# Optimization experiments

Hardware: AMD Instinct MI355X
Metric: run time of the kernel (lower is better)

## Reference

```python
import jax, jax.numpy as jnp
import numpy as np

N_NODES = 50000
N_EDGES = 800000
IN_CH = 128
HID = 32
HEADS = 8
OUT_CH = 40
NEG_SLOPE = 0.2


def setup_inputs() -> dict:
    key = jax.random.key(0)
    ks = jax.random.split(key, 12)
    g = lambda k, shape, fan: (jax.random.normal(k, shape, jnp.float32) / np.sqrt(fan).astype(np.float32))
    return {
        "x": jax.random.normal(ks[0], (N_NODES, IN_CH), jnp.float32),
        "edge_index": jax.random.randint(ks[1], (2, N_EDGES), 0, N_NODES, jnp.int64),
        "W1l": g(ks[2], (IN_CH, HEADS * HID), IN_CH),
        "W1r": g(ks[3], (IN_CH, HEADS * HID), IN_CH),
        "att1": g(ks[4], (HEADS, HID), HID),
        "b1": jnp.zeros((HEADS * HID,), jnp.float32),
        "W2l": g(ks[5], (HEADS * HID, HID), HEADS * HID),
        "W2r": g(ks[6], (HEADS * HID, HID), HEADS * HID),
        "att2": g(ks[7], (1, HID), HID),
        "b2": jnp.zeros((HID,), jnp.float32),
        "Wc": g(ks[8], (HID + IN_CH, OUT_CH), HID + IN_CH),
        "bc": jnp.zeros((OUT_CH,), jnp.float32),
    }


def _gatv2(x, ei, Wl, Wr, att, b, heads, ch):
    # GATv2Conv (concat=True): e_ij = att . LeakyReLU(Wl x_j + Wr x_i)
    n = x.shape[0]
    src, dst = ei[0], ei[1]  # message flows src(j) -> dst(i)
    xl = (x @ Wl).reshape(n, heads, ch)  # source transform
    xr = (x @ Wr).reshape(n, heads, ch)  # target transform
    e = jax.nn.leaky_relu(xl[src] + xr[dst], NEG_SLOPE)  # [E, H, C]
    score = jnp.einsum("ehc,hc->eh", e, att)             # [E, H]
    # per-target-node segment softmax (stable)
    m = jax.ops.segment_max(score, dst, num_segments=n)
    alpha = jnp.exp(score - m[dst])
    denom = jax.ops.segment_sum(alpha, dst, num_segments=n)
    alpha = alpha / denom[dst]
    out = jax.ops.segment_sum(alpha[:, :, None] * xl[src], dst, num_segments=n)
    return out.reshape(n, heads * ch) + b


def reference(x, edge_index, W1l, W1r, att1, b1, W2l, W2r, att2, b2, Wc, bc):
    n = x.shape[0]
    ar = jnp.arange(n, dtype=edge_index.dtype)
    ei = jnp.concatenate([edge_index, jnp.stack([ar, ar])], axis=1)  # add self-loops
    h1 = jax.nn.elu(_gatv2(x, ei, W1l, W1r, att1, b1, HEADS, HID))
    h2 = jax.nn.elu(_gatv2(h1, ei, W2l, W2r, att2, b2, 1, HID))
    combined = jnp.concatenate([h2, x], axis=1)
    return combined @ Wc + bc
```

## Files before the change

kernel.cpp:

```cpp
#include <hip/hip_runtime.h>
#include <cstdint>
#include <cstddef>
#include <math.h>

#define NN 50000
#define INCH 128
#define HIDC 32
#define NHEAD 8
#define OUTC 40

typedef unsigned short ushort_t;
using bf16x8 = __attribute__((ext_vector_type(8))) short;
using f32x4  = __attribute__((ext_vector_type(4))) float;

__device__ __forceinline__ float bf2f(unsigned short h) {
    return __uint_as_float(((unsigned int)h) << 16);
}
__device__ __forceinline__ unsigned short f2bf(float f) {
    unsigned int u = __float_as_uint(f);
    u = u + 0x7FFFu + ((u >> 16) & 1u);
    return (unsigned short)(u >> 16);
}
__device__ __forceinline__ float lo16(unsigned int u) { return __uint_as_float(u << 16); }
__device__ __forceinline__ float hi16(unsigned int u) { return __uint_as_float(u & 0xffff0000u); }

__global__ __launch_bounds__(256) void prep_all(
    const float* __restrict__ x, ushort_t* __restrict__ xb, int total8,
    const float* __restrict__ W1l, const float* __restrict__ W1r,
    const float* __restrict__ W2l, const float* __restrict__ W2r,
    const float* __restrict__ Wc,
    ushort_t* __restrict__ BT1, ushort_t* __restrict__ BT2, ushort_t* __restrict__ BTc,
    const int* __restrict__ ei, int E, int n, int* __restrict__ deg, int CX) {
    const int blk = blockIdx.x;
    const int tid = threadIdx.x;
    if (blk < CX) {
        int i = blk * 256 + tid;
        if (i >= total8) return;
        float4 f0 = *(const float4*)(x + (size_t)i * 8);
        float4 f1 = *(const float4*)(x + (size_t)i * 8 + 4);
        ushort4 u0, u1;
        u0.x = f2bf(f0.x); u0.y = f2bf(f0.y); u0.z = f2bf(f0.z); u0.w = f2bf(f0.w);
        u1.x = f2bf(f1.x); u1.y = f2bf(f1.y); u1.z = f2bf(f1.z); u1.w = f2bf(f1.w);
        *(ushort4*)(xb + (size_t)i * 8) = u0;
        *(ushort4*)(xb + (size_t)i * 8 + 4) = u1;
    } else if (blk < CX + 616) {
        int b = blk - CX, k = tid;
        if (b < 512) {
            if (k < 128) {
                float v = (b < 256) ? W1l[(size_t)k * 256 + b] : W1r[(size_t)k * 256 + (b - 256)];
                BT1[(size_t)b * 128 + k] = f2bf(v);
            }
        } else if (b < 576) {
            int c = b - 512;
            float v = (c < 32) ? W2l[(size_t)k * 32 + c] : W2r[(size_t)k * 32 + (c - 32)];
            BT2[(size_t)c * 256 + k] = f2bf(v);
        } else {
            int c = b - 576;
            if (k < 160) BTc[(size_t)c * 160 + k] = f2bf(Wc[(size_t)k * 40 + c]);
        }
    } else {
        int e = (blk - CX - 616) * 256 + tid;
        if (e >= E + n) return;
        int dst = (e < E) ? ei[E + e] : (e - E);
        atomicAdd(&deg[dst], 1);
    }
}


__global__ __launch_bounds__(1024) void partial_scan(
    const int* __restrict__ deg, int* __restrict__ row_start,
    int* __restrict__ block_total, int n) {
    __shared__ int wsum[16];
    const int tid = threadIdx.x, lane = tid & 63, wid = tid >> 6;
    int i = blockIdx.x * 1024 + tid;
    int v = (i < n) ? deg[i] : 0;
    int s = v;
    #pragma unroll
    for (int off = 1; off < 64; off <<= 1) {
        int t = __shfl_up(s, off, 64);
        if (lane >= off) s += t;
    }
    if (lane == 63) wsum[wid] = s;
    __syncthreads();
    if (wid == 0) {
        int ws = (lane < 16) ? wsum[lane] : 0;
        #pragma unroll
        for (int off = 1; off < 16; off <<= 1) {
            int t = __shfl_up(ws, off, 64);
            if (lane >= off) ws += t;
        }
        if (lane < 16) wsum[lane] = ws;
    }
    __syncthreads();
    int wexcl = wid ? wsum[wid - 1] : 0;
    if (i < n) row_start[i] = wexcl + s - v;
    if (tid == 0) block_total[blockIdx.x] = wsum[15];
}

__global__ void totals_scan(const int* __restrict__ block_total, int* __restrict__ block_off,
                            int* __restrict__ row_start_n, int nb) {
    int j = threadIdx.x;
    int v = (j < nb) ? block_total[j] : 0;
    int s = v;
    #pragma unroll
    for (int off = 1; off < 64; off <<= 1) {
        int t = __shfl_up(s, off, 64);
        if (j >= off) s += t;
    }
    if (j < nb) block_off[j] = s - v;
    if (j == nb - 1) *row_start_n = s;
}

__global__ __launch_bounds__(1024) void add_off(int* __restrict__ row_start, int* __restrict__ cursor,
                                                const int* __restrict__ block_off, int n) {
    int i = blockIdx.x * 1024 + threadIdx.x;
    if (i >= n) return;
    int val = row_start[i] + block_off[blockIdx.x];
    row_start[i] = val;
    cursor[i] = val;
}

__global__ void scatter_edges(const int* __restrict__ ei, int E, int n,
                              int* __restrict__ cursor, int* __restrict__ csr_src) {
    int e = blockIdx.x * blockDim.x + threadIdx.x;
    if (e >= E + n) return;
    int src, dst;
    if (e < E) { src = ei[e]; dst = ei[E + e]; } else { src = dst = e - E; }
    int pos = atomicAdd(&cursor[dst], 1);
    csr_src[pos] = src;
}

__global__ __launch_bounds__(256) void gemm1_mfma(
    const ushort_t* __restrict__ xb, const ushort_t* __restrict__ BT1,
    const float* __restrict__ att,
    ushort_t* __restrict__ xlr1, float* __restrict__ dl, float* __restrict__ dr, int M) {
    __shared__ ushort_t As[128][72];
    __shared__ ushort_t Bs[128][72];
    const int tid = threadIdx.x;
    const int rowBase = blockIdx.y * 128;
    const int bx = blockIdx.x;
    const int c0 = bx * 128;
    const int wid = tid >> 6, lane = tid & 63;
    const int wr = wid >> 1, wc = wid & 1;
    const int l15 = lane & 15, l4 = lane >> 4;
    f32x4 acc[4][4];
    #pragma unroll
    for (int i = 0; i < 4; ++i)
        #pragma unroll
        for (int j = 0; j < 4; ++j)
            #pragma unroll
            for (int q = 0; q < 4; ++q) acc[i][j][q] = 0.f;

    for (int c = 0; c < 2; ++c) {
        #pragma unroll
        for (int h = 0; h < 4; ++h) {
            int idx = h * 256 + tid;
            int r = idx >> 3, seg = idx & 7;
            int row = rowBase + r;
            uint4 v = {0, 0, 0, 0};
            if (row < M) v = *(const uint4*)(xb + (size_t)row * 128 + c * 64 + seg * 8);
            *(uint4*)&As[r][seg * 8] = v;
            *(uint4*)&Bs[r][seg * 8] = *(const uint4*)(BT1 + (size_t)(c0 + r) * 128 + c * 64 + seg * 8);
        }
        __syncthreads();
        #pragma unroll
        for (int kk = 0; kk < 2; ++kk) {
            bf16x8 a[4], b[4];
            #pragma unroll
            for (int f = 0; f < 4; ++f) {
                a[f] = *(const bf16x8*)&As[wr * 64 + f * 16 + l15][kk * 32 + l4 * 8];
                b[f] = *(const bf16x8*)&Bs[wc * 64 + f * 16 + l15][kk * 32 + l4 * 8];
            }
            #pragma unroll
            for (int i = 0; i < 4; ++i)
                #pragma unroll
                for (int j = 0; j < 4; ++j)
                    acc[i][j] = __builtin_amdgcn_mfma_f32_16x16x32_bf16(a[i], b[j], acc[i][j], 0, 0, 0);
        }
        __syncthreads();
    }
    #pragma unroll
    for (int i = 0; i < 4; ++i)
        #pragma unroll
        for (int r = 0; r < 4; ++r) {
            int row = rowBase + wr * 64 + i * 16 + l4 * 4 + r;
            if (row >= M) continue;
            #pragma unroll
            for (int j = 0; j < 4; ++j) {
                int col = c0 + wc * 64 + j * 16 + l15;
                xlr1[(size_t)row * 512 + col] = f2bf(acc[i][j][r]);
            }
        }
    float attv[4];
    #pragma unroll
    for (int j = 0; j < 4; ++j)
        attv[j] = att[(bx & 1) * 128 + wc * 64 + j * 16 + l15];
    float* __restrict__ dst = (bx < 2) ? dl : dr;
    const int headA = (bx & 1) * 4 + wc * 2;
    #pragma unroll
    for (int i = 0; i < 4; ++i)
        #pragma unroll
        for (int r = 0; r < 4; ++r) {
            float s0 = fmaf(acc[i][1][r], attv[1], acc[i][0][r] * attv[0]);
            float s1 = fmaf(acc[i][3][r], attv[3], acc[i][2][r] * attv[2]);
            s0 += __shfl_xor(s0, 1); s1 += __shfl_xor(s1, 1);
            s0 += __shfl_xor(s0, 2); s1 += __shfl_xor(s1, 2);
            s0 += __shfl_xor(s0, 4); s1 += __shfl_xor(s1, 4);
            s0 += __shfl_xor(s0, 8); s1 += __shfl_xor(s1, 8);
            if (l15 == 0) {
                int row = rowBase + wr * 64 + i * 16 + l4 * 4 + r;
                if (row < M) {
                    dst[(size_t)row * 8 + headA] = s0;
                    dst[(size_t)row * 8 + headA + 1] = s1;
                }
            }
        }
}

__global__ __launch_bounds__(256) void gat_agg1(
    const ushort_t* __restrict__ xlr, const float* __restrict__ dl,
    const float* __restrict__ dr, const float* __restrict__ att,
    const float* __restrict__ b,
    const int* __restrict__ row_start, const int* __restrict__ csr_src,
    ushort_t* __restrict__ h1) {
    const int lane = threadIdx.x & 63;
    const int i = blockIdx.x * 4 + (threadIdx.x >> 6);
    const int half = lane >> 5;
    const int sl = lane & 31;
    const int head = sl >> 2;

    uint4 xv = *(const uint4*)(xlr + (size_t)i * 512 + 256 + sl * 8);
    const float xr0 = lo16(xv.x), xr1 = hi16(xv.x), xr2 = lo16(xv.y), xr3 = hi16(xv.y);
    const float xr4 = lo16(xv.z), xr5 = hi16(xv.z), xr6 = lo16(xv.w), xr7 = hi16(xv.w);
    const float4 atA = *(const float4*)(att + sl * 8);
    const float4 atB = *(const float4*)(att + sl * 8 + 4);
    const float cbase = 0.6f * dr[(size_t)i * 8 + head];
    const int p0 = row_start[i], p1 = row_start[i + 1];

    float d = 0.f;
    float a0 = 0.f, a1 = 0.f, a2 = 0.f, a3 = 0.f, a4 = 0.f, a5 = 0.f, a6 = 0.f, a7 = 0.f;

    int e0 = p0 + half;     int pc0 = e0 < p1 ? e0 : p1 - 1;
    int j0 = csr_src[pc0];
    uint4 uv0 = *(const uint4*)(xlr + (size_t)j0 * 512 + sl * 8);
    float dl0 = dl[(size_t)j0 * 8 + head];
    int e1 = p0 + half + 2; int pc1 = e1 < p1 ? e1 : p1 - 1;
    int j1 = csr_src[pc1];
    uint4 uv1 = *(const uint4*)(xlr + (size_t)j1 * 512 + sl * 8);
    float dl1 = dl[(size_t)j1 * 8 + head];

    for (int p = p0; p < p1; p += 4) {
        {
            const bool val = (p + half) < p1;
            float v0 = lo16(uv0.x), v1 = hi16(uv0.x), v2 = lo16(uv0.y), v3 = hi16(uv0.y);
            float v4 = lo16(uv0.z), v5 = hi16(uv0.z), v6 = lo16(uv0.w), v7 = hi16(uv0.w);
            float base = fmaf(0.6f, dl0, cbase);
            int nxt = p + half + 4;
            if (nxt < p1) {
                int jn = csr_src[nxt];
                uv0 = *(const uint4*)(xlr + (size_t)jn * 512 + sl * 8);
                dl0 = dl[(size_t)jn * 8 + head];
            }
            float q = atA.x * fabsf(v0 + xr0);
            q = fmaf(atA.y, fabsf(v1 + xr1), q);
            q = fmaf(atA.z, fabsf(v2 + xr2), q);
            q = fmaf(atA.w, fabsf(v3 + xr3), q);
            q = fmaf(atB.x, fabsf(v4 + xr4), q);
            q = fmaf(atB.y, fabsf(v5 + xr5), q);
            q = fmaf(atB.z, fabsf(v6 + xr6), q);
            q = fmaf(atB.w, fabsf(v7 + xr7), q);
            q += __shfl_xor(q, 1);
            q += __shfl_xor(q, 2);
            float w = val ? __expf(fmaf(0.4f, q, base)) : 0.f;
            d += w;
            a0 = fmaf(w, v0, a0); a1 = fmaf(w, v1, a1);
            a2 = fmaf(w, v2, a2); a3 = fmaf(w, v3, a3);
            a4 = fmaf(w, v4, a4); a5 = fmaf(w, v5, a5);
            a6 = fmaf(w, v6, a6); a7 = fmaf(w, v7, a7);
        }
        {
            const bool val = (p + 2 + half) < p1;
            float v0 = lo16(uv1.x), v1 = hi16(uv1.x), v2 = lo16(uv1.y), v3 = hi16(uv1.y);
            float v4 = lo16(uv1.z), v5 = hi16(uv1.z), v6 = lo16(uv1.w), v7 = hi16(uv1.w);
            float base = fmaf(0.6f, dl1, cbase);
            int nxt = p + half + 6;
            if (nxt < p1) {
                int jn = csr_src[nxt];
                uv1 = *(const uint4*)(xlr + (size_t)jn * 512 + sl * 8);
                dl1 = dl[(size_t)jn * 8 + head];
            }
            float q = atA.x * fabsf(v0 + xr0);
            q = fmaf(atA.y, fabsf(v1 + xr1), q);
            q = fmaf(atA.z, fabsf(v2 + xr2), q);
            q = fmaf(atA.w, fabsf(v3 + xr3), q);
            q = fmaf(atB.x, fabsf(v4 + xr4), q);
            q = fmaf(atB.y, fabsf(v5 + xr5), q);
            q = fmaf(atB.z, fabsf(v6 + xr6), q);
            q = fmaf(atB.w, fabsf(v7 + xr7), q);
            q += __shfl_xor(q, 1);
            q += __shfl_xor(q, 2);
            float w = val ? __expf(fmaf(0.4f, q, base)) : 0.f;
            d += w;
            a0 = fmaf(w, v0, a0); a1 = fmaf(w, v1, a1);
            a2 = fmaf(w, v2, a2); a3 = fmaf(w, v3, a3);
            a4 = fmaf(w, v4, a4); a5 = fmaf(w, v5, a5);
            a6 = fmaf(w, v6, a6); a7 = fmaf(w, v7, a7);
        }
    }
    d  += __shfl_xor(d, 32);
    a0 += __shfl_xor(a0, 32); a1 += __shfl_xor(a1, 32);
    a2 += __shfl_xor(a2, 32); a3 += __shfl_xor(a3, 32);
    a4 += __shfl_xor(a4, 32); a5 += __shfl_xor(a5, 32);
    a6 += __shfl_xor(a6, 32); a7 += __shfl_xor(a7, 32);

    if (half == 0) {
        const float4 bA = *(const float4*)(b + sl * 8);
        const float4 bB = *(const float4*)(b + sl * 8 + 4);
        float inv = 1.f / d;
        float o0 = fmaf(a0, inv, bA.x), o1 = fmaf(a1, inv, bA.y);
        float o2 = fmaf(a2, inv, bA.z), o3 = fmaf(a3, inv, bA.w);
        float o4 = fmaf(a4, inv, bB.x), o5 = fmaf(a5, inv, bB.y);
        float o6 = fmaf(a6, inv, bB.z), o7 = fmaf(a7, inv, bB.w);
        o0 = o0 > 0.f ? o0 : __expf(o0) - 1.f;
        o1 = o1 > 0.f ? o1 : __expf(o1) - 1.f;
        o2 = o2 > 0.f ? o2 : __expf(o2) - 1.f;
        o3 = o3 > 0.f ? o3 : __expf(o3) - 1.f;
        o4 = o4 > 0.f ? o4 : __expf(o4) - 1.f;
        o5 = o5 > 0.f ? o5 : __expf(o5) - 1.f;
        o6 = o6 > 0.f ? o6 : __expf(o6) - 1.f;
        o7 = o7 > 0.f ? o7 : __expf(o7) - 1.f;
        uint4 ov;
        ov.x = ((unsigned)f2bf(o1) << 16) | f2bf(o0);
        ov.y = ((unsigned)f2bf(o3) << 16) | f2bf(o2);
        ov.z = ((unsigned)f2bf(o5) << 16) | f2bf(o4);
        ov.w = ((unsigned)f2bf(o7) << 16) | f2bf(o6);
        *(uint4*)(h1 + (size_t)i * 256 + sl * 8) = ov;
    }
}

__global__ __launch_bounds__(256) void gemm2_mfma(
    const ushort_t* __restrict__ h1, const ushort_t* __restrict__ BT2,
    const float* __restrict__ att,
    ushort_t* __restrict__ xlr2, float* __restrict__ dl2, float* __restrict__ dr2, int M) {
    __shared__ ushort_t As[128][72];
    __shared__ ushort_t Bs[64][264];
    const int tid = threadIdx.x;
    const int rowBase = blockIdx.x * 128;
    const int wid = tid >> 6, lane = tid & 63;
    const int l15 = lane & 15, l4 = lane >> 4;
    #pragma unroll
    for (int h = 0; h < 8; ++h) {
        int idx = h * 256 + tid;
        int r = idx >> 5, seg = idx & 31;
        *(uint4*)&Bs[r][seg * 8] = *(const uint4*)(BT2 + (size_t)r * 256 + seg * 8);
    }
    f32x4 acc[2][4];
    #pragma unroll
    for (int i = 0; i < 2; ++i)
        #pragma unroll
        for (int j = 0; j < 4; ++j)
            #pragma unroll
            for (int q = 0; q < 4; ++q) acc[i][j][q] = 0.f;

    for (int c = 0; c < 4; ++c) {
        #pragma unroll
        for (int h = 0; h < 4; ++h) {
            int idx = h * 256 + tid;
            int r = idx >> 3, seg = idx & 7;
            int row = rowBase + r;
            uint4 v = {0, 0, 0, 0};
            if (row < M) v = *(const uint4*)(h1 + (size_t)row * 256 + c * 64 + seg * 8);
            *(uint4*)&As[r][seg * 8] = v;
        }
        __syncthreads();
        #pragma unroll
        for (int kk = 0; kk < 2; ++kk) {
            bf16x8 a[2], b[4];
            #pragma unroll
            for (int f = 0; f < 2; ++f)
                a[f] = *(const bf16x8*)&As[wid * 32 + f * 16 + l15][kk * 32 + l4 * 8];
            #pragma unroll
            for (int f = 0; f < 4; ++f)
                b[f] = *(const bf16x8*)&Bs[f * 16 + l15][c * 64 + kk * 32 + l4 * 8];
            #pragma unroll
            for (int i = 0; i < 2; ++i)
                #pragma unroll
                for (int j = 0; j < 4; ++j)
                    acc[i][j] = __builtin_amdgcn_mfma_f32_16x16x32_bf16(a[i], b[j], acc[i][j], 0, 0, 0);
        }
        __syncthreads();
    }
    #pragma unroll
    for (int i = 0; i < 2; ++i)
        #pragma unroll
        for (int r = 0; r < 4; ++r) {
            int row = rowBase + wid * 32 + i * 16 + l4 * 4 + r;
            if (row >= M) continue;
            #pragma unroll
            for (int j = 0; j < 4; ++j) {
                int col = j * 16 + l15;
                xlr2[(size_t)row * 64 + col] = f2bf(acc[i][j][r]);
            }
        }
    float attv[4];
    #pragma unroll
    for (int j = 0; j < 4; ++j)
        attv[j] = att[(j * 16 + l15) & 31];
    #pragma unroll
    for (int i = 0; i < 2; ++i)
        #pragma unroll
        for (int r = 0; r < 4; ++r) {
            float s0 = fmaf(acc[i][1][r], attv[1], acc[i][0][r] * attv[0]);
            float s1 = fmaf(acc[i][3][r], attv[3], acc[i][2][r] * attv[2]);
            s0 += __shfl_xor(s0, 1); s1 += __shfl_xor(s1, 1);
            s0 += __shfl_xor(s0, 2); s1 += __shfl_xor(s1, 2);
            s0 += __shfl_xor(s0, 4); s1 += __shfl_xor(s1, 4);
            s0 += __shfl_xor(s0, 8); s1 += __shfl_xor(s1, 8);
            if (l15 == 0) {
                int row = rowBase + wid * 32 + i * 16 + l4 * 4 + r;
                if (row < M) {
                    dl2[row] = s0;
                    dr2[row] = s1;
                }
            }
        }
}

__global__ __launch_bounds__(256) void gat_agg2(
    const ushort_t* __restrict__ xlr, const float* __restrict__ dl,
    const float* __restrict__ dr, const float* __restrict__ att,
    const float* __restrict__ b,
    const int* __restrict__ row_start, const int* __restrict__ csr_src,
    ushort_t* __restrict__ h2) {
    const int lane = threadIdx.x & 63;
    const int i = blockIdx.x * 4 + (threadIdx.x >> 6);
    const int g = lane >> 3;
    const int h8 = lane & 7;
    uint2 xv = *(const uint2*)(xlr + (size_t)i * 64 + 32 + h8 * 4);
    const float xr0 = lo16(xv.x), xr1 = hi16(xv.x), xr2 = lo16(xv.y), xr3 = hi16(xv.y);
    const float4 at = *(const float4*)(att + h8 * 4);
    const float cbase = 0.6f * dr[i];
    const int p0 = row_start[i], p1 = row_start[i + 1];
    float d = 0.f, a0 = 0.f, a1 = 0.f, a2 = 0.f, a3 = 0.f;

    int e0 = p0 + g;     int pc0 = e0 < p1 ? e0 : p1 - 1;
    int j0 = csr_src[pc0];
    uint2 uv0 = *(const uint2*)(xlr + (size_t)j0 * 64 + h8 * 4);
    float dl0 = dl[j0];
    int e1 = p0 + g + 8; int pc1 = e1 < p1 ? e1 : p1 - 1;
    int j1 = csr_src[pc1];
    uint2 uv1 = *(const uint2*)(xlr + (size_t)j1 * 64 + h8 * 4);
    float dl1 = dl[j1];

    for (int p = p0; p < p1; p += 16) {
        {
            const bool val = (p + g) < p1;
            float v0 = lo16(uv0.x), v1 = hi16(uv0.x), v2 = lo16(uv0.y), v3 = hi16(uv0.y);
            float base = fmaf(0.6f, dl0, cbase);
            int nxt = p + g + 16;
            if (nxt < p1) {
                int jn = csr_src[nxt];
                uv0 = *(const uint2*)(xlr + (size_t)jn * 64 + h8 * 4);
                dl0 = dl[jn];
            }
            float q = at.x * fabsf(v0 + xr0);
            q = fmaf(at.y, fabsf(v1 + xr1), q);
            q = fmaf(at.z, fabsf(v2 + xr2), q);
            q = fmaf(at.w, fabsf(v3 + xr3), q);
            q += __shfl_xor(q, 1);
            q += __shfl_xor(q, 2);
            q += __shfl_xor(q, 4);
            float w = val ? __expf(fmaf(0.4f, q, base)) : 0.f;
            d += w;
            a0 = fmaf(w, v0, a0); a1 = fmaf(w, v1, a1);
            a2 = fmaf(w, v2, a2); a3 = fmaf(w, v3, a3);
        }
        {
            const bool val = (p + g + 8) < p1;
            float v0 = lo16(uv1.x), v1 = hi16(uv1.x), v2 = lo16(uv1.y), v3 = hi16(uv1.y);
            float base = fmaf(0.6f, dl1, cbase);
            int nxt = p + g + 24;
            if (nxt < p1) {
                int jn = csr_src[nxt];
                uv1 = *(const uint2*)(xlr + (size_t)jn * 64 + h8 * 4);
                dl1 = dl[jn];
            }
            float q = at.x * fabsf(v0 + xr0);
            q = fmaf(at.y, fabsf(v1 + xr1), q);
            q = fmaf(at.z, fabsf(v2 + xr2), q);
            q = fmaf(at.w, fabsf(v3 + xr3), q);
            q += __shfl_xor(q, 1);
            q += __shfl_xor(q, 2);
            q += __shfl_xor(q, 4);
            float w = val ? __expf(fmaf(0.4f, q, base)) : 0.f;
            d += w;
            a0 = fmaf(w, v0, a0); a1 = fmaf(w, v1, a1);
            a2 = fmaf(w, v2, a2); a3 = fmaf(w, v3, a3);
        }
    }
    d  += __shfl_xor(d, 8);  d  += __shfl_xor(d, 16);  d  += __shfl_xor(d, 32);
    a0 += __shfl_xor(a0, 8); a0 += __shfl_xor(a0, 16); a0 += __shfl_xor(a0, 32);
    a1 += __shfl_xor(a1, 8); a1 += __shfl_xor(a1, 16); a1 += __shfl_xor(a1, 32);
    a2 += __shfl_xor(a2, 8); a2 += __shfl_xor(a2, 16); a2 += __shfl_xor(a2, 32);
    a3 += __shfl_xor(a3, 8); a3 += __shfl_xor(a3, 16); a3 += __shfl_xor(a3, 32);
    if (g == 0) {
        const float4 bb = *(const float4*)(b + h8 * 4);
        float inv = 1.f / d;
        float o0 = fmaf(a0, inv, bb.x);
        float o1 = fmaf(a1, inv, bb.y);
        float o2 = fmaf(a2, inv, bb.z);
        float o3 = fmaf(a3, inv, bb.w);
        o0 = o0 > 0.f ? o0 : __expf(o0) - 1.f;
        o1 = o1 > 0.f ? o1 : __expf(o1) - 1.f;
        o2 = o2 > 0.f ? o2 : __expf(o2) - 1.f;
        o3 = o3 > 0.f ? o3 : __expf(o3) - 1.f;
        uint2 ov;
        ov.x = ((unsigned)f2bf(o1) << 16) | f2bf(o0);
        ov.y = ((unsigned)f2bf(o3) << 16) | f2bf(o2);
        *(uint2*)(h2 + (size_t)i * 32 + h8 * 4) = ov;
    }
}

__global__ __launch_bounds__(256) void final_mfma(
    const ushort_t* __restrict__ h2, const ushort_t* __restrict__ xb,
    const ushort_t* __restrict__ BTc, const float* __restrict__ bc,
    float* __restrict__ out, int M) {
    __shared__ ushort_t As[128][168];
    __shared__ ushort_t Bs[48][168];
    const int tid = threadIdx.x;
    const int rowBase = blockIdx.x * 128;
    const int wid = tid >> 6, lane = tid & 63;
    const int l15 = lane & 15, l4 = lane >> 4;
    #pragma unroll
    for (int h = 0; h < 4; ++h) {
        int idx = h * 256 + tid;
        if (idx < 960) {
            int r = idx / 20, seg = idx % 20;
            uint4 v = {0, 0, 0, 0};
            if (r < 40) v = *(const uint4*)(BTc + (size_t)r * 160 + seg * 8);
            *(uint4*)&Bs[r][seg * 8] = v;
        }
    }
    #pragma unroll
    for (int h = 0; h < 10; ++h) {
        int idx = h * 256 + tid;
        int r = idx / 20, seg = idx % 20;
        int row = rowBase + r;
        uint4 v = {0, 0, 0, 0};
        if (row < M)
            v = (seg < 4) ? *(const uint4*)(h2 + (size_t)row * 32 + seg * 8)
                          : *(const uint4*)(xb + (size_t)row * 128 + (seg - 4) * 8);
        *(uint4*)&As[r][seg * 8] = v;
    }
    __syncthreads();
    f32x4 acc[2][3];
    #pragma unroll
    for (int i = 0; i < 2; ++i)
        #pragma unroll
        for (int j = 0; j < 3; ++j)
            #pragma unroll
            for (int q = 0; q < 4; ++q) acc[i][j][q] = 0.f;
    #pragma unroll
    for (int kk = 0; kk < 5; ++kk) {
        bf16x8 a[2], b[3];
        #pragma unroll
        for (int f = 0; f < 2; ++f)
            a[f] = *(const bf16x8*)&As[wid * 32 + f * 16 + l15][kk * 32 + l4 * 8];
        #pragma unroll
        for (int f = 0; f < 3; ++f)
            b[f] = *(const bf16x8*)&Bs[f * 16 + l15][kk * 32 + l4 * 8];
        #pragma unroll
        for (int i = 0; i < 2; ++i)
            #pragma unroll
            for (int j = 0; j < 3; ++j)
                acc[i][j] = __builtin_amdgcn_mfma_f32_16x16x32_bf16(a[i], b[j], acc[i][j], 0, 0, 0);
    }
    #pragma unroll
    for (int i = 0; i < 2; ++i)
        #pragma unroll
        for (int r = 0; r < 4; ++r) {
            int row = rowBase + wid * 32 + i * 16 + l4 * 4 + r;
            if (row >= M) continue;
            #pragma unroll
            for (int j = 0; j < 3; ++j) {
                int col = j * 16 + l15;
                if (col < 40) out[(size_t)row * 40 + col] = acc[i][j][r] + bc[col];
            }
        }
}


extern "C" void kernel_launch(void* const* d_in, const int* in_sizes, int n_in,
                              void* d_out, int out_size, void* d_ws, size_t ws_size,
                              hipStream_t stream) {
    const float* x    = (const float*)d_in[0];
    const int*   ei   = (const int*)d_in[1];
    const float* W1l  = (const float*)d_in[2];
    const float* W1r  = (const float*)d_in[3];
    const float* att1 = (const float*)d_in[4];
    const float* b1   = (const float*)d_in[5];
    const float* W2l  = (const float*)d_in[6];
    const float* W2r  = (const float*)d_in[7];
    const float* att2 = (const float*)d_in[8];
    const float* b2   = (const float*)d_in[9];
    const float* Wc   = (const float*)d_in[10];
    const float* bc   = (const float*)d_in[11];
    float* out = (float*)d_out;

    const int n  = NN;
    const int E  = in_sizes[1] / 2;
    const int TE = E + n;
    const int NB = (n + 1023) / 1024;
    const int CX = (n * 128 / 8 + 255) / 256;
    const int CD = (TE + 255) / 256;

    char* ws = (char*)d_ws;
    size_t off = 0;
    auto alloc = [&](size_t bytes) { void* p = ws + off; off += (bytes + 255) & ~(size_t)255; return p; };
    ushort_t* xb   = (ushort_t*)alloc((size_t)n * 128 * 2);
    ushort_t* xlr1 = (ushort_t*)alloc((size_t)n * 512 * 2);
    ushort_t* h1   = (ushort_t*)alloc((size_t)n * 256 * 2);
    ushort_t* xlr2 = (ushort_t*)alloc((size_t)n * 64 * 2);
    ushort_t* h2   = (ushort_t*)alloc((size_t)n * 32 * 2);
    ushort_t* BT1  = (ushort_t*)alloc(512 * 128 * 2);
    ushort_t* BT2  = (ushort_t*)alloc(64 * 256 * 2);
    ushort_t* BTc  = (ushort_t*)alloc(40 * 160 * 2);
    float* dl1 = (float*)alloc((size_t)n * 8 * 4);
    float* dr1 = (float*)alloc((size_t)n * 8 * 4);
    float* dl2 = (float*)alloc((size_t)n * 4);
    float* dr2 = (float*)alloc((size_t)n * 4);
    int* row_start   = (int*)alloc((size_t)(n + 1) * 4);
    int* cursor      = (int*)alloc((size_t)(n + 1) * 4);
    int* deg         = (int*)alloc((size_t)n * 4);
    int* block_total = (int*)alloc((size_t)NB * 4);
    int* block_off   = (int*)alloc((size_t)NB * 4);
    int* csr_src     = (int*)alloc((size_t)TE * 4);

    hipMemsetAsync(deg, 0, (size_t)n * 4, stream);
    prep_all<<<CX + 616 + CD, 256, 0, stream>>>(x, xb, n * 128 / 8,
        W1l, W1r, W2l, W2r, Wc, BT1, BT2, BTc, ei, E, n, deg, CX);

    partial_scan<<<NB, 1024, 0, stream>>>(deg, row_start, block_total, n);
    totals_scan<<<1, 64, 0, stream>>>(block_total, block_off, row_start + n, NB);
    add_off<<<NB, 1024, 0, stream>>>(row_start, cursor, block_off, n);
    scatter_edges<<<CD, 256, 0, stream>>>(ei, E, n, cursor, csr_src);

    gemm1_mfma<<<dim3(4, (n + 127) / 128), 256, 0, stream>>>(xb, BT1, att1, xlr1, dl1, dr1, n);
    gat_agg1<<<n / 4, 256, 0, stream>>>(xlr1, dl1, dr1, att1, b1, row_start, csr_src, h1);

    gemm2_mfma<<<(n + 127) / 128, 256, 0, stream>>>(h1, BT2, att2, xlr2, dl2, dr2, n);
    gat_agg2<<<n / 4, 256, 0, stream>>>(xlr2, dl2, dr2, att2, b2, row_start, csr_src, h2);

    final_mfma<<<(n + 127) / 128, 256, 0, stream>>>(h2, xb, BTc, bc, out, n);
}
```

Before: 342.9 us.

## Remap lanes in GAT aggregation kernels and deepen gather prefetch

In layer-1 aggregation, each wavefront now processes one edge at a time across all 64 lanes, with 4 channels per lane. Previously two half-waves each took 8 channels per lane. An 8-deep register ring prefetches neighbor rows and removes the cross-half reduction at the end. In layer-2 aggregation, lanes cover 2 channels each with 4 edge groups in flight instead of 8 groups of 4 channels, again with a 4-deep prefetch ring. The aim is to raise memory-level parallelism and simplify reductions, at the cost of narrower per-lane loads, more shuffle steps per edge and more serialized edge iterations per wave.

```diff
diff --git a/kernel.cpp b/kernel.cpp
--- a/kernel.cpp
+++ b/kernel.cpp
@@ -225,117 +225,64 @@
     ushort_t* __restrict__ h1) {
     const int lane = threadIdx.x & 63;
     const int i = blockIdx.x * 4 + (threadIdx.x >> 6);
-    const int half = lane >> 5;
-    const int sl = lane & 31;
-    const int head = sl >> 2;
-
-    uint4 xv = *(const uint4*)(xlr + (size_t)i * 512 + 256 + sl * 8);
+    const int head = lane >> 3;
+
+    uint2 xv = *(const uint2*)(xlr + (size_t)i * 512 + 256 + lane * 4);
     const float xr0 = lo16(xv.x), xr1 = hi16(xv.x), xr2 = lo16(xv.y), xr3 = hi16(xv.y);
-    const float xr4 = lo16(xv.z), xr5 = hi16(xv.z), xr6 = lo16(xv.w), xr7 = hi16(xv.w);
-    const float4 atA = *(const float4*)(att + sl * 8);
-    const float4 atB = *(const float4*)(att + sl * 8 + 4);
+    const float4 at = *(const float4*)(att + lane * 4);
     const float cbase = 0.6f * dr[(size_t)i * 8 + head];
     const int p0 = row_start[i], p1 = row_start[i + 1];
 
-    float d = 0.f;
-    float a0 = 0.f, a1 = 0.f, a2 = 0.f, a3 = 0.f, a4 = 0.f, a5 = 0.f, a6 = 0.f, a7 = 0.f;
-
-    int e0 = p0 + half;     int pc0 = e0 < p1 ? e0 : p1 - 1;
-    int j0 = csr_src[pc0];
-    uint4 uv0 = *(const uint4*)(xlr + (size_t)j0 * 512 + sl * 8);
-    float dl0 = dl[(size_t)j0 * 8 + head];
-    int e1 = p0 + half + 2; int pc1 = e1 < p1 ? e1 : p1 - 1;
-    int j1 = csr_src[pc1];
-    uint4 uv1 = *(const uint4*)(xlr + (size_t)j1 * 512 + sl * 8);
-    float dl1 = dl[(size_t)j1 * 8 + head];
-
-    for (int p = p0; p < p1; p += 4) {
-        {
-            const bool val = (p + half) < p1;
-            float v0 = lo16(uv0.x), v1 = hi16(uv0.x), v2 = lo16(uv0.y), v3 = hi16(uv0.y);
-            float v4 = lo16(uv0.z), v5 = hi16(uv0.z), v6 = lo16(uv0.w), v7 = hi16(uv0.w);
-            float base = fmaf(0.6f, dl0, cbase);
-            int nxt = p + half + 4;
+    float d = 0.f, a0 = 0.f, a1 = 0.f, a2 = 0.f, a3 = 0.f;
+
+    uint2 uv[8];
+    float dlv[8];
+    #pragma unroll
+    for (int s = 0; s < 8; ++s) {
+        int pc = p0 + s; pc = pc < p1 ? pc : p1 - 1;
+        int j = csr_src[pc];
+        uv[s] = *(const uint2*)(xlr + (size_t)j * 512 + lane * 4);
+        dlv[s] = dl[(size_t)j * 8 + head];
+    }
+
+    for (int p = p0; p < p1; p += 8) {
+        #pragma unroll
+        for (int s = 0; s < 8; ++s) {
+            const bool val = (p + s) < p1;
+            float v0 = lo16(uv[s].x), v1 = hi16(uv[s].x);
+            float v2 = lo16(uv[s].y), v3 = hi16(uv[s].y);
+            float base = fmaf(0.6f, dlv[s], cbase);
+            int nxt = p + s + 8;
             if (nxt < p1) {
-                int jn = csr_src[nxt];
-                uv0 = *(const uint4*)(xlr + (size_t)jn * 512 + sl * 8);
-                dl0 = dl[(size_t)jn * 8 + head];
-            }
-            float q = atA.x * fabsf(v0 + xr0);
-            q = fmaf(atA.y, fabsf(v1 + xr1), q);
-            q = fmaf(atA.z, fabsf(v2 + xr2), q);
-            q = fmaf(atA.w, fabsf(v3 + xr3), q);
-            q = fmaf(atB.x, fabsf(v4 + xr4), q);
-            q = fmaf(atB.y, fabsf(v5 + xr5), q);
-            q = fmaf(atB.z, fabsf(v6 + xr6), q);
-            q = fmaf(atB.w, fabsf(v7 + xr7), q);
+                int j = csr_src[nxt];
+                uv[s] = *(const uint2*)(xlr + (size_t)j * 512 + lane * 4);
+                dlv[s] = dl[(size_t)j * 8 + head];
+            }
+            float q = at.x * fabsf(v0 + xr0);
+            q = fmaf(at.y, fabsf(v1 + xr1), q);
+            q = fmaf(at.z, fabsf(v2 + xr2), q);
+            q = fmaf(at.w, fabsf(v3 + xr3), q);
             q += __shfl_xor(q, 1);
             q += __shfl_xor(q, 2);
+            q += __shfl_xor(q, 4);
             float w = val ? __expf(fmaf(0.4f, q, base)) : 0.f;
             d += w;
             a0 = fmaf(w, v0, a0); a1 = fmaf(w, v1, a1);
             a2 = fmaf(w, v2, a2); a3 = fmaf(w, v3, a3);
-            a4 = fmaf(w, v4, a4); a5 = fmaf(w, v5, a5);
-            a6 = fmaf(w, v6, a6); a7 = fmaf(w, v7, a7);
-        }
-        {
-            const bool val = (p + 2 + half) < p1;
-            float v0 = lo16(uv1.x), v1 = hi16(uv1.x), v2 = lo16(uv1.y), v3 = hi16(uv1.y);
-            float v4 = lo16(uv1.z), v5 = hi16(uv1.z), v6 = lo16(uv1.w), v7 = hi16(uv1.w);
-            float base = fmaf(0.6f, dl1, cbase);
-            int nxt = p + half + 6;
-            if (nxt < p1) {
-                int jn = csr_src[nxt];
-                uv1 = *(const uint4*)(xlr + (size_t)jn * 512 + sl * 8);
-                dl1 = dl[(size_t)jn * 8 + head];
-            }
-            float q = atA.x * fabsf(v0 + xr0);
-            q = fmaf(atA.y, fabsf(v1 + xr1), q);
-            q = fmaf(atA.z, fabsf(v2 + xr2), q);
-            q = fmaf(atA.w, fabsf(v3 + xr3), q);
-            q = fmaf(atB.x, fabsf(v4 + xr4), q);
-            q = fmaf(atB.y, fabsf(v5 + xr5), q);
-            q = fmaf(atB.z, fabsf(v6 + xr6), q);
-            q = fmaf(atB.w, fabsf(v7 + xr7), q);
-            q += __shfl_xor(q, 1);
-            q += __shfl_xor(q, 2);
-            float w = val ? __expf(fmaf(0.4f, q, base)) : 0.f;
-            d += w;
-            a0 = fmaf(w, v0, a0); a1 = fmaf(w, v1, a1);
-            a2 = fmaf(w, v2, a2); a3 = fmaf(w, v3, a3);
-            a4 = fmaf(w, v4, a4); a5 = fmaf(w, v5, a5);
-            a6 = fmaf(w, v6, a6); a7 = fmaf(w, v7, a7);
-        }
-    }
-    d  += __shfl_xor(d, 32);
-    a0 += __shfl_xor(a0, 32); a1 += __shfl_xor(a1, 32);
-    a2 += __shfl_xor(a2, 32); a3 += __shfl_xor(a3, 32);
-    a4 += __shfl_xor(a4, 32); a5 += __shfl_xor(a5, 32);
-    a6 += __shfl_xor(a6, 32); a7 += __shfl_xor(a7, 32);
-
-    if (half == 0) {
-        const float4 bA = *(const float4*)(b + sl * 8);
-        const float4 bB = *(const float4*)(b + sl * 8 + 4);
-        float inv = 1.f / d;
-        float o0 = fmaf(a0, inv, bA.x), o1 = fmaf(a1, inv, bA.y);
-        float o2 = fmaf(a2, inv, bA.z), o3 = fmaf(a3, inv, bA.w);
-        float o4 = fmaf(a4, inv, bB.x), o5 = fmaf(a5, inv, bB.y);
-        float o6 = fmaf(a6, inv, bB.z), o7 = fmaf(a7, inv, bB.w);
-        o0 = o0 > 0.f ? o0 : __expf(o0) - 1.f;
-        o1 = o1 > 0.f ? o1 : __expf(o1) - 1.f;
-        o2 = o2 > 0.f ? o2 : __expf(o2) - 1.f;
-        o3 = o3 > 0.f ? o3 : __expf(o3) - 1.f;
-        o4 = o4 > 0.f ? o4 : __expf(o4) - 1.f;
-        o5 = o5 > 0.f ? o5 : __expf(o5) - 1.f;
-        o6 = o6 > 0.f ? o6 : __expf(o6) - 1.f;
-        o7 = o7 > 0.f ? o7 : __expf(o7) - 1.f;
-        uint4 ov;
-        ov.x = ((unsigned)f2bf(o1) << 16) | f2bf(o0);
-        ov.y = ((unsigned)f2bf(o3) << 16) | f2bf(o2);
-        ov.z = ((unsigned)f2bf(o5) << 16) | f2bf(o4);
-        ov.w = ((unsigned)f2bf(o7) << 16) | f2bf(o6);
-        *(uint4*)(h1 + (size_t)i * 256 + sl * 8) = ov;
-    }
+        }
+    }
+    const float4 bb = *(const float4*)(b + lane * 4);
+    float inv = 1.f / d;
+    float o0 = fmaf(a0, inv, bb.x), o1 = fmaf(a1, inv, bb.y);
+    float o2 = fmaf(a2, inv, bb.z), o3 = fmaf(a3, inv, bb.w);
+    o0 = o0 > 0.f ? o0 : __expf(o0) - 1.f;
+    o1 = o1 > 0.f ? o1 : __expf(o1) - 1.f;
+    o2 = o2 > 0.f ? o2 : __expf(o2) - 1.f;
+    o3 = o3 > 0.f ? o3 : __expf(o3) - 1.f;
+    uint2 ov;
+    ov.x = ((unsigned)f2bf(o1) << 16) | f2bf(o0);
+    ov.y = ((unsigned)f2bf(o3) << 16) | f2bf(o2);
+    *(uint2*)(h1 + (size_t)i * 256 + lane * 4) = ov;
 }
 
 __global__ __launch_bounds__(256) void gemm2_mfma(
@@ -434,90 +381,60 @@
     ushort_t* __restrict__ h2) {
     const int lane = threadIdx.x & 63;
     const int i = blockIdx.x * 4 + (threadIdx.x >> 6);
-    const int g = lane >> 3;
-    const int h8 = lane & 7;
-    uint2 xv = *(const uint2*)(xlr + (size_t)i * 64 + 32 + h8 * 4);
-    const float xr0 = lo16(xv.x), xr1 = hi16(xv.x), xr2 = lo16(xv.y), xr3 = hi16(xv.y);
-    const float4 at = *(const float4*)(att + h8 * 4);
+    const int g = lane >> 4;
+    const int h = lane & 15;
+    const unsigned xru = *(const unsigned*)(xlr + (size_t)i * 64 + 32 + h * 2);
+    const float xr0 = lo16(xru), xr1v = hi16(xru);
+    const float2 atv = *(const float2*)(att + h * 2);
     const float cbase = 0.6f * dr[i];
     const int p0 = row_start[i], p1 = row_start[i + 1];
-    float d = 0.f, a0 = 0.f, a1 = 0.f, a2 = 0.f, a3 = 0.f;
-
-    int e0 = p0 + g;     int pc0 = e0 < p1 ? e0 : p1 - 1;
-    int j0 = csr_src[pc0];
-    uint2 uv0 = *(const uint2*)(xlr + (size_t)j0 * 64 + h8 * 4);
-    float dl0 = dl[j0];
-    int e1 = p0 + g + 8; int pc1 = e1 < p1 ? e1 : p1 - 1;
-    int j1 = csr_src[pc1];
-    uint2 uv1 = *(const uint2*)(xlr + (size_t)j1 * 64 + h8 * 4);
-    float dl1 = dl[j1];
+    float d = 0.f, a0 = 0.f, a1 = 0.f;
+
+    unsigned uv[4];
+    float dlv[4];
+    #pragma unroll
+    for (int s = 0; s < 4; ++s) {
+        int pc = p0 + s * 4 + g; pc = pc < p1 ? pc : p1 - 1;
+        int j = csr_src[pc];
+        uv[s] = *(const unsigned*)(xlr + (size_t)j * 64 + h * 2);
+        dlv[s] = dl[j];
+    }
 
     for (int p = p0; p < p1; p += 16) {
-        {
-            const bool val = (p + g) < p1;
-            float v0 = lo16(uv0.x), v1 = hi16(uv0.x), v2 = lo16(uv0.y), v3 = hi16(uv0.y);
-            float base = fmaf(0.6f, dl0, cbase);
-            int nxt = p + g + 16;
+        #pragma unroll
+        for (int s = 0; s < 4; ++s) {
+            const bool val = (p + s * 4 + g) < p1;
+            float v0 = lo16(uv[s]), v1 = hi16(uv[s]);
+            float base = fmaf(0.6f, dlv[s], cbase);
+            int nxt = p + s * 4 + g + 16;
             if (nxt < p1) {
-                int jn = csr_src[nxt];
-                uv0 = *(const uint2*)(xlr + (size_t)jn * 64 + h8 * 4);
-                dl0 = dl[jn];
-            }
-            float q = at.x * fabsf(v0 + xr0);
-            q = fmaf(at.y, fabsf(v1 + xr1), q);
-            q = fmaf(at.z, fabsf(v2 + xr2), q);
-            q = fmaf(at.w, fabsf(v3 + xr3), q);
+                int j = csr_src[nxt];
+                uv[s] = *(const unsigned*)(xlr + (size_t)j * 64 + h * 2);
+                dlv[s] = dl[j];
+            }
+            float q = atv.x * fabsf(v0 + xr0);
+            q = fmaf(atv.y, fabsf(v1 + xr1v), q);
             q += __shfl_xor(q, 1);
             q += __shfl_xor(q, 2);
             q += __shfl_xor(q, 4);
+            q += __shfl_xor(q, 8);
             float w = val ? __expf(fmaf(0.4f, q, base)) : 0.f;
             d += w;
-            a0 = fmaf(w, v0, a0); a1 = fmaf(w, v1, a1);
-            a2 = fmaf(w, v2, a2); a3 = fmaf(w, v3, a3);
-        }
-        {
-            const bool val = (p + g + 8) < p1;
-            float v0 = lo16(uv1.x), v1 = hi16(uv1.x), v2 = lo16(uv1.y), v3 = hi16(uv1.y);
-            float base = fmaf(0.6f, dl1, cbase);
-            int nxt = p + g + 24;
-            if (nxt < p1) {
-                int jn = csr_src[nxt];
-                uv1 = *(const uint2*)(xlr + (size_t)jn * 64 + h8 * 4);
-                dl1 = dl[jn];
-            }
-            float q = at.x * fabsf(v0 + xr0);
-            q = fmaf(at.y, fabsf(v1 + xr1), q);
-            q = fmaf(at.z, fabsf(v2 + xr2), q);
-            q = fmaf(at.w, fabsf(v3 + xr3), q);
-            q += __shfl_xor(q, 1);
-            q += __shfl_xor(q, 2);
-            q += __shfl_xor(q, 4);
-            float w = val ? __expf(fmaf(0.4f, q, base)) : 0.f;
-            d += w;
-            a0 = fmaf(w, v0, a0); a1 = fmaf(w, v1, a1);
-            a2 = fmaf(w, v2, a2); a3 = fmaf(w, v3, a3);
-        }
-    }
-    d  += __shfl_xor(d, 8);  d  += __shfl_xor(d, 16);  d  += __shfl_xor(d, 32);
-    a0 += __shfl_xor(a0, 8); a0 += __shfl_xor(a0, 16); a0 += __shfl_xor(a0, 32);
-    a1 += __shfl_xor(a1, 8); a1 += __shfl_xor(a1, 16); a1 += __shfl_xor(a1, 32);
-    a2 += __shfl_xor(a2, 8); a2 += __shfl_xor(a2, 16); a2 += __shfl_xor(a2, 32);
-    a3 += __shfl_xor(a3, 8); a3 += __shfl_xor(a3, 16); a3 += __shfl_xor(a3, 32);
+            a0 = fmaf(w, v0, a0);
+            a1 = fmaf(w, v1, a1);
+        }
+    }
+    d  += __shfl_xor(d, 16);  d  += __shfl_xor(d, 32);
+    a0 += __shfl_xor(a0, 16); a0 += __shfl_xor(a0, 32);
+    a1 += __shfl_xor(a1, 16); a1 += __shfl_xor(a1, 32);
     if (g == 0) {
-        const float4 bb = *(const float4*)(b + h8 * 4);
         float inv = 1.f / d;
-        float o0 = fmaf(a0, inv, bb.x);
-        float o1 = fmaf(a1, inv, bb.y);
-        float o2 = fmaf(a2, inv, bb.z);
-        float o3 = fmaf(a3, inv, bb.w);
+        float o0 = fmaf(a0, inv, b[h * 2]);
+        float o1 = fmaf(a1, inv, b[h * 2 + 1]);
         o0 = o0 > 0.f ? o0 : __expf(o0) - 1.f;
         o1 = o1 > 0.f ? o1 : __expf(o1) - 1.f;
-        o2 = o2 > 0.f ? o2 : __expf(o2) - 1.f;
-        o3 = o3 > 0.f ? o3 : __expf(o3) - 1.f;
-        uint2 ov;
-        ov.x = ((unsigned)f2bf(o1) << 16) | f2bf(o0);
-        ov.y = ((unsigned)f2bf(o3) << 16) | f2bf(o2);
-        *(uint2*)(h2 + (size_t)i * 32 + h8 * 4) = ov;
+        ushort2 ou; ou.x = f2bf(o0); ou.y = f2bf(o1);
+        *(ushort2*)(h2 + (size_t)i * 32 + h * 2) = ou;
     }
 }
 
```

After: 434.1 us. 26.6% more time.
